# Kernel tuning notes

Hardware: AMD Instinct MI355X
Metric: run time of the kernel (lower is better)

Reference implementation:

```python
import jax, jax.numpy as jnp
import numpy as np

NUM_HEADS = 64
HEAD_DIM = 10  # forced by nn.Linear(10, 1)


def setup_inputs() -> dict:
    key = jax.random.key(0)
    kq, kk, kv, kw = jax.random.split(key, 4)
    B, T, M = 16, 4096, NUM_HEADS * HEAD_DIM
    return {
        "query": jax.random.normal(kq, (B, T, M), dtype=jnp.float32),
        "key": jax.random.normal(kk, (B, T, M), dtype=jnp.float32),
        "value": jax.random.normal(kv, (B, T, M), dtype=jnp.float32),
        "W": jax.random.normal(kw, (1, HEAD_DIM), dtype=jnp.float32) * 0.3,
        "b": jnp.zeros((1,), dtype=jnp.float32),
    }


def _to_heads(x):
    # torch: stack(split(x, head_dim, dim=2), dim=0) -> [H, B, T, D]
    B, T, M = x.shape
    return x.reshape(B, T, NUM_HEADS, HEAD_DIM).transpose(2, 0, 1, 3)


def reference(query, key, value, W, b):
    D = HEAD_DIM
    q = _to_heads(query)   # [H,B,T,D]
    k = _to_heads(key)     # [H,B,T,D]
    v = _to_heads(value)   # [H,B,T,D]
    # key.transpose(-1,-2).sum(3).unsqueeze(2): sum over T -> [H,B,1,D]
    k_sum = k.sum(axis=2, keepdims=True)
    attn = jax.nn.softmax(jnp.tanh(q * k_sum / np.float32(np.sqrt(D))), axis=-1)
    t = attn * v                          # [H,B,T,D]
    v_q = t.sum(axis=2)                   # [H,B,D]
    v_v = t.sum(axis=3).transpose(1, 0, 2)  # [B,H,T]
    # input_proj: Linear(10,1) on v_q*v_q (v_query == v_key == t summed over T)
    s = jnp.tanh((v_q * v_q) @ W.T + b)   # [H,B,1]
    s = jax.nn.softmax(s, axis=-1)        # softmax over size-1 dim (== ones)
    s = s.transpose(1, 0, 2)              # [B,H,1]
    return v_v * s                        # [B,H,T]
```

## Files before the change

### kernel.cpp

```cpp
#include <hip/hip_runtime.h>

#define BB 16
#define TT 4096
#define HH 64
#define DD 10
#define MM 640

#define TROWS 16
#define PADF  161

__global__ void zero_ws_kernel(float* __restrict__ ws, int n) {
    int i = blockIdx.x * blockDim.x + threadIdx.x;
    if (i < n) ws[i] = 0.0f;
}

__global__ void __launch_bounds__(256)
ksum_kernel(const float* __restrict__ key, float* __restrict__ ksum) {
    int g = blockIdx.x * blockDim.x + threadIdx.x;
    int b = g / 160;
    int c = g % 160;
    int t0 = blockIdx.y * 32;

    const float4* p = reinterpret_cast<const float4*>(key)
                    + (size_t)b * TT * 160 + (size_t)t0 * 160 + c;

    float4 a0 = make_float4(0.f,0.f,0.f,0.f);
    float4 a1 = make_float4(0.f,0.f,0.f,0.f);
    float4 a2 = make_float4(0.f,0.f,0.f,0.f);
    float4 a3 = make_float4(0.f,0.f,0.f,0.f);
    #pragma unroll
    for (int i = 0; i < 32; i += 4) {
        float4 x0 = p[(size_t)(i + 0) * 160];
        float4 x1 = p[(size_t)(i + 1) * 160];
        float4 x2 = p[(size_t)(i + 2) * 160];
        float4 x3 = p[(size_t)(i + 3) * 160];
        a0.x += x0.x; a0.y += x0.y; a0.z += x0.z; a0.w += x0.w;
        a1.x += x1.x; a1.y += x1.y; a1.z += x1.z; a1.w += x1.w;
        a2.x += x2.x; a2.y += x2.y; a2.z += x2.z; a2.w += x2.w;
        a3.x += x3.x; a3.y += x3.y; a3.z += x3.z; a3.w += x3.w;
    }
    float sx = (a0.x + a1.x) + (a2.x + a3.x);
    float sy = (a0.y + a1.y) + (a2.y + a3.y);
    float sz = (a0.z + a1.z) + (a2.z + a3.z);
    float sw = (a0.w + a1.w) + (a2.w + a3.w);

    float* dst = ksum + b * MM + c * 4;
    atomicAdd(dst + 0, sx);
    atomicAdd(dst + 1, sy);
    atomicAdd(dst + 2, sz);
    atomicAdd(dst + 3, sw);
}

__device__ __forceinline__ float tanh_fast(float x) {
    float ax = fabsf(x);
    float e2 = __expf(-2.0f * ax);
    float th = (1.0f - e2) / (1.0f + e2);
    return copysignf(th, x);
}

__global__ void __launch_bounds__(128)
attn_kernel(const float* __restrict__ q,
            const float* __restrict__ v,
            const float* __restrict__ ksum,
            float* __restrict__ out) {
    __shared__ float qs[TROWS * PADF];
    __shared__ float vs[TROWS * PADF];

    const int tid = threadIdx.x;
    const int t0  = blockIdx.x * TROWS;
    const int hg  = blockIdx.y;
    const int b   = blockIdx.z;

    const float4* qg = reinterpret_cast<const float4*>(q)
                     + ((size_t)(b * TT + t0)) * 160 + hg * 40;
    const float4* vg = reinterpret_cast<const float4*>(v)
                     + ((size_t)(b * TT + t0)) * 160 + hg * 40;

    float4 rq[5], rv[5];
    #pragma unroll
    for (int i = 0; i < 5; ++i) {
        int idx = tid + 128 * i;
        int row = idx / 40;
        int c   = idx % 40;
        rq[i] = qg[(size_t)row * 160 + c];
        rv[i] = vg[(size_t)row * 160 + c];
    }
    #pragma unroll
    for (int i = 0; i < 5; ++i) {
        int idx  = tid + 128 * i;
        int row  = idx / 40;
        int c    = idx % 40;
        int base = row * PADF + c * 4;
        qs[base + 0] = rq[i].x; qs[base + 1] = rq[i].y;
        qs[base + 2] = rq[i].z; qs[base + 3] = rq[i].w;
        vs[base + 0] = rv[i].x; vs[base + 1] = rv[i].y;
        vs[base + 2] = rv[i].z; vs[base + 3] = rv[i].w;
    }
    __syncthreads();

    const float R = 0.316227766016838f;
    #pragma unroll
    for (int o = 0; o < 2; ++o) {
        int p    = tid + o * 128;
        int row  = p & (TROWS - 1);
        int head = p >> 4;
        const float* ks = ksum + b * MM + hg * 160 + head * 10;

        int lbase = row * PADF + head * 10;
        float sum = 0.f, dot = 0.f;
        #pragma unroll
        for (int d = 0; d < 10; ++d) {
            float e = __expf(tanh_fast(qs[lbase + d] * ks[d] * R));
            sum += e;
            dot += e * vs[lbase + d];
        }
        out[((size_t)(b * HH + hg * 16 + head)) * TT + t0 + row] = dot / sum;
    }
}

extern "C" void kernel_launch(void* const* d_in, const int* in_sizes, int n_in,
                              void* d_out, int out_size, void* d_ws, size_t ws_size,
                              hipStream_t stream) {
    const float* q = (const float*)d_in[0];
    const float* k = (const float*)d_in[1];
    const float* v = (const float*)d_in[2];
    float* out  = (float*)d_out;
    float* ksum = (float*)d_ws;

    zero_ws_kernel<<<dim3((BB * MM + 255) / 256), dim3(256), 0, stream>>>(ksum, BB * MM);
    ksum_kernel<<<dim3(10, 128), dim3(256), 0, stream>>>(k, ksum);
    attn_kernel<<<dim3(TT / TROWS, 4, BB), dim3(128), 0, stream>>>(q, v, ksum, out);
}
```

Before: 115.8 us.

## Make attention kernel persistent with register prefetch of next tile

Turns the attention kernel into a persistent grid of a fixed number of blocks that loop over tiles. Each block prefetches the next tile's q/v into registers while it computes the current one. Shared memory is now stored as float4 rows, ksum is loaded as float2, and divisions become hardware reciprocals. The aim is to overlap global loads with compute and cut launch/tail overhead, in exchange for an extra barrier per tile and lower occupancy from held registers.

```diff
diff --git a/kernel.cpp b/kernel.cpp
--- a/kernel.cpp
+++ b/kernel.cpp
@@ -7,7 +7,9 @@
 #define MM 640
 
 #define TROWS 16
-#define PADF  161
+#define PADF4 41
+#define NBLK 1792
+#define NTILE (256 * 4 * BB)
 
 __global__ void zero_ws_kernel(float* __restrict__ ws, int n) {
     int i = blockIdx.x * blockDim.x + threadIdx.x;
@@ -51,10 +53,10 @@
     atomicAdd(dst + 3, sw);
 }
 
-__device__ __forceinline__ float tanh_fast(float x) {
+__device__ __forceinline__ float tanh_rcp(float x) {
     float ax = fabsf(x);
     float e2 = __expf(-2.0f * ax);
-    float th = (1.0f - e2) / (1.0f + e2);
+    float th = (1.0f - e2) * __builtin_amdgcn_rcpf(1.0f + e2);
     return copysignf(th, x);
 }
 
@@ -63,58 +65,96 @@
             const float* __restrict__ v,
             const float* __restrict__ ksum,
             float* __restrict__ out) {
-    __shared__ float qs[TROWS * PADF];
-    __shared__ float vs[TROWS * PADF];
+    __shared__ float4 qs[TROWS * PADF4];
+    __shared__ float4 vs[TROWS * PADF4];
 
     const int tid = threadIdx.x;
-    const int t0  = blockIdx.x * TROWS;
-    const int hg  = blockIdx.y;
-    const int b   = blockIdx.z;
+    const int bid = blockIdx.x;
 
-    const float4* qg = reinterpret_cast<const float4*>(q)
-                     + ((size_t)(b * TT + t0)) * 160 + hg * 40;
-    const float4* vg = reinterpret_cast<const float4*>(v)
-                     + ((size_t)(b * TT + t0)) * 160 + hg * 40;
-
-    float4 rq[5], rv[5];
+    int rows[5], cols[5];
     #pragma unroll
     for (int i = 0; i < 5; ++i) {
         int idx = tid + 128 * i;
-        int row = idx / 40;
-        int c   = idx % 40;
-        rq[i] = qg[(size_t)row * 160 + c];
-        rv[i] = vg[(size_t)row * 160 + c];
+        rows[i] = idx / 40;
+        cols[i] = idx % 40;
     }
-    #pragma unroll
-    for (int i = 0; i < 5; ++i) {
-        int idx  = tid + 128 * i;
-        int row  = idx / 40;
-        int c    = idx % 40;
-        int base = row * PADF + c * 4;
-        qs[base + 0] = rq[i].x; qs[base + 1] = rq[i].y;
-        qs[base + 2] = rq[i].z; qs[base + 3] = rq[i].w;
-        vs[base + 0] = rv[i].x; vs[base + 1] = rv[i].y;
-        vs[base + 2] = rv[i].z; vs[base + 3] = rv[i].w;
-    }
-    __syncthreads();
+    const int head0 = tid >> 4;
+    const int row   = tid & 15;
 
     const float R = 0.316227766016838f;
-    #pragma unroll
-    for (int o = 0; o < 2; ++o) {
-        int p    = tid + o * 128;
-        int row  = p & (TROWS - 1);
-        int head = p >> 4;
-        const float* ks = ksum + b * MM + hg * 160 + head * 10;
 
-        int lbase = row * PADF + head * 10;
-        float sum = 0.f, dot = 0.f;
+    float4 rq[5], rv[5];
+    {
+        int t0 = (bid & 255) * TROWS;
+        int hg = (bid >> 8) & 3;
+        int b  = bid >> 10;
+        const float4* qg = reinterpret_cast<const float4*>(q)
+                         + ((size_t)(b * TT + t0)) * 160 + hg * 40;
+        const float4* vg = reinterpret_cast<const float4*>(v)
+                         + ((size_t)(b * TT + t0)) * 160 + hg * 40;
         #pragma unroll
-        for (int d = 0; d < 10; ++d) {
-            float e = __expf(tanh_fast(qs[lbase + d] * ks[d] * R));
-            sum += e;
-            dot += e * vs[lbase + d];
+        for (int i = 0; i < 5; ++i) {
+            rq[i] = qg[(size_t)rows[i] * 160 + cols[i]];
+            rv[i] = vg[(size_t)rows[i] * 160 + cols[i]];
         }
-        out[((size_t)(b * HH + hg * 16 + head)) * TT + t0 + row] = dot / sum;
+    }
+
+    for (int vt = bid; vt < NTILE; vt += NBLK) {
+        const int t0 = (vt & 255) * TROWS;
+        const int hg = (vt >> 8) & 3;
+        const int b  = vt >> 10;
+
+        const float* ks0 = ksum + b * MM + hg * 160 + head0 * 10;
+        const float* ks1 = ks0 + 80;
+        float2 kk0[5], kk1[5];
+        #pragma unroll
+        for (int i = 0; i < 5; ++i) {
+            kk0[i] = *reinterpret_cast<const float2*>(ks0 + 2 * i);
+            kk1[i] = *reinterpret_cast<const float2*>(ks1 + 2 * i);
+        }
+
+        __syncthreads();
+        #pragma unroll
+        for (int i = 0; i < 5; ++i) {
+            qs[rows[i] * PADF4 + cols[i]] = rq[i];
+            vs[rows[i] * PADF4 + cols[i]] = rv[i];
+        }
+        __syncthreads();
+
+        int vn = vt + NBLK;
+        if (vn < NTILE) {
+            int t0n = (vn & 255) * TROWS;
+            int hgn = (vn >> 8) & 3;
+            int bn  = vn >> 10;
+            const float4* qg = reinterpret_cast<const float4*>(q)
+                             + ((size_t)(bn * TT + t0n)) * 160 + hgn * 40;
+            const float4* vg = reinterpret_cast<const float4*>(v)
+                             + ((size_t)(bn * TT + t0n)) * 160 + hgn * 40;
+            #pragma unroll
+            for (int i = 0; i < 5; ++i) {
+                rq[i] = qg[(size_t)rows[i] * 160 + cols[i]];
+                rv[i] = vg[(size_t)rows[i] * 160 + cols[i]];
+            }
+        }
+
+        const float* qsf = reinterpret_cast<const float*>(qs);
+        const float* vsf = reinterpret_cast<const float*>(vs);
+        #pragma unroll
+        for (int o = 0; o < 2; ++o) {
+            const int head  = head0 + o * 8;
+            const int lbase = row * (PADF4 * 4) + head * 10;
+            const float2* kk = o ? kk1 : kk0;
+            float sum = 0.f, dot = 0.f;
+            #pragma unroll
+            for (int i = 0; i < 5; ++i) {
+                float e0 = __expf(tanh_rcp(qsf[lbase + 2*i]     * kk[i].x * R));
+                float e1 = __expf(tanh_rcp(qsf[lbase + 2*i + 1] * kk[i].y * R));
+                sum += e0 + e1;
+                dot += e0 * vsf[lbase + 2*i] + e1 * vsf[lbase + 2*i + 1];
+            }
+            out[((size_t)(b * HH + hg * 16 + head)) * TT + t0 + row]
+                = dot * __builtin_amdgcn_rcpf(sum);
+        }
     }
 }
 
@@ -129,5 +169,5 @@
 
     zero_ws_kernel<<<dim3((BB * MM + 255) / 256), dim3(256), 0, stream>>>(ksum, BB * MM);
     ksum_kernel<<<dim3(10, 128), dim3(256), 0, stream>>>(k, ksum);
-    attn_kernel<<<dim3(TT / TROWS, 4, BB), dim3(128), 0, stream>>>(q, v, ksum, out);
+    attn_kernel<<<dim3(NBLK), dim3(128), 0, stream>>>(q, v, ksum, out);
 }
```

Result: slower. 200.2 us (+72.8%).

## Make attention kernel persistent with double-buffered async global-to-LDS loads

Applied to the files above, without the earlier changes.

Replaces the one-tile-per-block attention kernel with 2048 persistent single-wave blocks. Each block loops over 8-row time tiles and double-buffers q and v tiles into LDS through global_load_lds async copies, using an XOR-swizzled layout to avoid bank conflicts. The ksum values are hoisted into registers once per block, and divisions are replaced with hardware reciprocals. The aim is to overlap memory fetch with compute and cut per-block launch and sync overhead. In exchange it relies on hand-placed vmcnt waits and there is no barrier between the waves' LDS use (single wave, so it holds).

```diff
diff --git a/kernel.cpp b/kernel.cpp
--- a/kernel.cpp
+++ b/kernel.cpp
@@ -1,13 +1,15 @@
 #include <hip/hip_runtime.h>
+#include <stdint.h>
 
 #define BB 16
 #define TT 4096
 #define HH 64
-#define DD 10
 #define MM 640
 
-#define TROWS 16
-#define PADF  161
+#define TROWS 8
+#define NTT   (TT / TROWS)
+#define SUBS  32
+#define NBLK  (64 * SUBS)
 
 __global__ void zero_ws_kernel(float* __restrict__ ws, int n) {
     int i = blockIdx.x * blockDim.x + threadIdx.x;
@@ -51,70 +53,109 @@
     atomicAdd(dst + 3, sw);
 }
 
-__device__ __forceinline__ float tanh_fast(float x) {
+__device__ __forceinline__ float tanh_rcp(float x) {
     float ax = fabsf(x);
     float e2 = __expf(-2.0f * ax);
-    float th = (1.0f - e2) / (1.0f + e2);
+    float th = (1.0f - e2) * __builtin_amdgcn_rcpf(1.0f + e2);
     return copysignf(th, x);
 }
 
-__global__ void __launch_bounds__(128)
+__device__ __forceinline__ void async_cp16(const float4* g, void* l) {
+    __builtin_amdgcn_global_load_lds(
+        (const __attribute__((address_space(1))) uint32_t*)g,
+        (__attribute__((address_space(3))) uint32_t*)l,
+        16, 0, 0);
+}
+
+__global__ void __launch_bounds__(64)
 attn_kernel(const float* __restrict__ q,
             const float* __restrict__ v,
             const float* __restrict__ ksum,
             float* __restrict__ out) {
-    __shared__ float qs[TROWS * PADF];
-    __shared__ float vs[TROWS * PADF];
+    __shared__ float4 lds[2][640];
 
-    const int tid = threadIdx.x;
-    const int t0  = blockIdx.x * TROWS;
-    const int hg  = blockIdx.y;
-    const int b   = blockIdx.z;
+    const int lane = threadIdx.x;
+    const int bid  = blockIdx.x;
+    const int sub   = bid & (SUBS - 1);
+    const int combo = bid >> 5;
+    const int b  = combo >> 2;
+    const int hg = combo & 3;
 
-    const float4* qg = reinterpret_cast<const float4*>(q)
-                     + ((size_t)(b * TT + t0)) * 160 + hg * 40;
-    const float4* vg = reinterpret_cast<const float4*>(v)
-                     + ((size_t)(b * TT + t0)) * 160 + hg * 40;
-
-    float4 rq[5], rv[5];
+    int srcoff[5];
     #pragma unroll
     for (int i = 0; i < 5; ++i) {
-        int idx = tid + 128 * i;
-        int row = idx / 40;
-        int c   = idx % 40;
-        rq[i] = qg[(size_t)row * 160 + c];
-        rv[i] = vg[(size_t)row * 160 + c];
+        int s = i * 64 + lane;
+        int r = s / 40;
+        srcoff[i] = r * 160 + ((s % 40) ^ r);
     }
-    #pragma unroll
-    for (int i = 0; i < 5; ++i) {
-        int idx  = tid + 128 * i;
-        int row  = idx / 40;
-        int c    = idx % 40;
-        int base = row * PADF + c * 4;
-        qs[base + 0] = rq[i].x; qs[base + 1] = rq[i].y;
-        qs[base + 2] = rq[i].z; qs[base + 3] = rq[i].w;
-        vs[base + 0] = rv[i].x; vs[base + 1] = rv[i].y;
-        vs[base + 2] = rv[i].z; vs[base + 3] = rv[i].w;
-    }
-    __syncthreads();
+
+    const int row   = lane & 7;
+    const int head0 = lane >> 3;
+
+    const float4* qbase = (const float4*)q + (size_t)b * TT * 160 + hg * 40;
+    const float4* vbase = (const float4*)v + (size_t)b * TT * 160 + hg * 40;
 
     const float R = 0.316227766016838f;
+    float ksr[2][10];
     #pragma unroll
     for (int o = 0; o < 2; ++o) {
-        int p    = tid + o * 128;
-        int row  = p & (TROWS - 1);
-        int head = p >> 4;
-        const float* ks = ksum + b * MM + hg * 160 + head * 10;
+        const float* ks = ksum + b * MM + hg * 160 + (head0 + 8 * o) * 10;
+        #pragma unroll
+        for (int d = 0; d < 10; ++d) ksr[o][d] = ks[d] * R;
+    }
 
-        int lbase = row * PADF + head * 10;
-        float sum = 0.f, dot = 0.f;
+    float* obase0 = out + ((size_t)(b * HH + hg * 16 + head0)) * TT + row;
+    float* obase1 = obase0 + (size_t)8 * TT;
+
+    {
+        const float4* qt = qbase + (size_t)sub * 1280;
+        const float4* vt = vbase + (size_t)sub * 1280;
         #pragma unroll
-        for (int d = 0; d < 10; ++d) {
-            float e = __expf(tanh_fast(qs[lbase + d] * ks[d] * R));
-            sum += e;
-            dot += e * vs[lbase + d];
+        for (int i = 0; i < 5; ++i)
+            async_cp16(qt + srcoff[i], (char*)&lds[0][0] + i * 1024);
+        #pragma unroll
+        for (int i = 0; i < 5; ++i)
+            async_cp16(vt + srcoff[i], (char*)&lds[0][320] + i * 1024);
+    }
+
+    int buf = 0;
+    for (int tt = sub; tt < NTT; tt += SUBS) {
+        int ttn = tt + SUBS;
+        if (ttn < NTT) {
+            const float4* qt = qbase + (size_t)ttn * 1280;
+            const float4* vt = vbase + (size_t)ttn * 1280;
+            #pragma unroll
+            for (int i = 0; i < 5; ++i)
+                async_cp16(qt + srcoff[i], (char*)&lds[buf ^ 1][0] + i * 1024);
+            #pragma unroll
+            for (int i = 0; i < 5; ++i)
+                async_cp16(vt + srcoff[i], (char*)&lds[buf ^ 1][320] + i * 1024);
+            asm volatile("s_waitcnt vmcnt(10)" ::: "memory");
+        } else {
+            asm volatile("s_waitcnt vmcnt(0)" ::: "memory");
         }
-        out[((size_t)(b * HH + hg * 16 + head)) * TT + t0 + row] = dot / sum;
+        __builtin_amdgcn_sched_barrier(0);
+
+        const float* qf = (const float*)&lds[buf][0];
+        const float* vf = (const float*)&lds[buf][320];
+        const int rb = row * 160;
+        const int rx = row << 2;
+
+        #pragma unroll
+        for (int o = 0; o < 2; ++o) {
+            const int c0 = (head0 + 8 * o) * 10;
+            float sum = 0.f, dot = 0.f;
+            #pragma unroll
+            for (int d = 0; d < 10; ++d) {
+                int fi = rb + ((c0 + d) ^ rx);
+                float e = __expf(tanh_rcp(qf[fi] * ksr[o][d]));
+                sum += e;
+                dot += e * vf[fi];
+            }
+            float res = dot * __builtin_amdgcn_rcpf(sum);
+            (o ? obase1 : obase0)[(size_t)tt * TROWS] = res;
+        }
+        buf ^= 1;
     }
 }
 
@@ -129,5 +170,5 @@
 
     zero_ws_kernel<<<dim3((BB * MM + 255) / 256), dim3(256), 0, stream>>>(ksum, BB * MM);
     ksum_kernel<<<dim3(10, 128), dim3(256), 0, stream>>>(k, ksum);
-    attn_kernel<<<dim3(TT / TROWS, 4, BB), dim3(128), 0, stream>>>(q, v, ksum, out);
+    attn_kernel<<<dim3(NBLK), dim3(64), 0, stream>>>(q, v, ksum, out);
 }
```

Result: slower. 131.0 us (+13.1%).

## Make attention kernel persistent over time tiles with register-prefetch pipelining

Applied to the files above, without the earlier changes.

The attention kernel now launches 1024 blocks of 256 threads. Each block loops over 16 time tiles and prefetches the next tile of q and v into registers while it computes the current tile from shared memory. Each thread loads its ksum values once, pre-scaled, and divisions are replaced with rcp intrinsics. The workspace zero kernel becomes hipMemsetAsync. Fewer, longer blocks cut launch overhead and the repeated ksum loads, but lower parallelism and extra barriers may limit latency hiding.

```diff
diff --git a/kernel.cpp b/kernel.cpp
--- a/kernel.cpp
+++ b/kernel.cpp
@@ -1,18 +1,17 @@
 #include <hip/hip_runtime.h>
+#include <stdint.h>
 
 #define BB 16
 #define TT 4096
 #define HH 64
-#define DD 10
 #define MM 640
 
-#define TROWS 16
-#define PADF  161
-
-__global__ void zero_ws_kernel(float* __restrict__ ws, int n) {
-    int i = blockIdx.x * blockDim.x + threadIdx.x;
-    if (i < n) ws[i] = 0.0f;
-}
+#define PAD4  41
+#define ROWSF (PAD4 * 4)
+#define QVOFF (16 * ROWSF)
+#define NPART 16
+#define NITER 16
+#define NBLK  (64 * NPART)
 
 __global__ void __launch_bounds__(256)
 ksum_kernel(const float* __restrict__ key, float* __restrict__ ksum) {
@@ -51,70 +50,103 @@
     atomicAdd(dst + 3, sw);
 }
 
-__device__ __forceinline__ float tanh_fast(float x) {
+__device__ __forceinline__ float tanh_rcp(float x) {
     float ax = fabsf(x);
     float e2 = __expf(-2.0f * ax);
-    float th = (1.0f - e2) / (1.0f + e2);
+    float th = (1.0f - e2) * __builtin_amdgcn_rcpf(1.0f + e2);
     return copysignf(th, x);
 }
 
-__global__ void __launch_bounds__(128)
+__global__ void __launch_bounds__(256)
 attn_kernel(const float* __restrict__ q,
             const float* __restrict__ v,
             const float* __restrict__ ksum,
             float* __restrict__ out) {
-    __shared__ float qs[TROWS * PADF];
-    __shared__ float vs[TROWS * PADF];
+    __shared__ float sbuf[2 * 16 * ROWSF];
 
-    const int tid = threadIdx.x;
-    const int t0  = blockIdx.x * TROWS;
-    const int hg  = blockIdx.y;
-    const int b   = blockIdx.z;
+    const int tid   = threadIdx.x;
+    const int bid   = blockIdx.x;
+    const int combo = bid >> 4;
+    const int tpart = bid & (NPART - 1);
+    const int b  = combo >> 2;
+    const int hg = combo & 3;
 
-    const float4* qg = reinterpret_cast<const float4*>(q)
-                     + ((size_t)(b * TT + t0)) * 160 + hg * 40;
-    const float4* vg = reinterpret_cast<const float4*>(v)
-                     + ((size_t)(b * TT + t0)) * 160 + hg * 40;
-
-    float4 rq[5], rv[5];
+    int sr[5], sc[5], qsel[5];
     #pragma unroll
     for (int i = 0; i < 5; ++i) {
-        int idx = tid + 128 * i;
-        int row = idx / 40;
-        int c   = idx % 40;
-        rq[i] = qg[(size_t)row * 160 + c];
-        rv[i] = vg[(size_t)row * 160 + c];
+        int idx = tid + 256 * i;
+        int qq  = (idx < 640) ? 1 : 0;
+        int s   = qq ? idx : (idx - 640);
+        sr[i] = s / 40;
+        sc[i] = s % 40;
+        qsel[i] = qq;
+    }
+
+    const int row  = tid & 15;
+    const int head = tid >> 4;
+
+    const float R = 0.316227766016838f;
+    float ksr[10];
+    {
+        const float* ks = ksum + b * MM + hg * 160 + head * 10;
+        #pragma unroll
+        for (int d = 0; d < 10; ++d) ksr[d] = ks[d] * R;
+    }
+
+    const float4* qb4 = (const float4*)q + (size_t)b * TT * 160 + hg * 40;
+    const float4* vb4 = (const float4*)v + (size_t)b * TT * 160 + hg * 40;
+    float* ob = out + ((size_t)(b * HH + hg * 16 + head)) * TT + row;
+
+    float4  rs[5];
+    float4* s4 = (float4*)sbuf;
+    const int tbase = tpart * (NITER * 16);
+
+    #pragma unroll
+    for (int i = 0; i < 5; ++i) {
+        const float4* base = qsel[i] ? qb4 : vb4;
+        rs[i] = base[(size_t)(tbase + sr[i]) * 160 + sc[i]];
     }
     #pragma unroll
-    for (int i = 0; i < 5; ++i) {
-        int idx  = tid + 128 * i;
-        int row  = idx / 40;
-        int c    = idx % 40;
-        int base = row * PADF + c * 4;
-        qs[base + 0] = rq[i].x; qs[base + 1] = rq[i].y;
-        qs[base + 2] = rq[i].z; qs[base + 3] = rq[i].w;
-        vs[base + 0] = rv[i].x; vs[base + 1] = rv[i].y;
-        vs[base + 2] = rv[i].z; vs[base + 3] = rv[i].w;
-    }
-    __syncthreads();
+    for (int i = 0; i < 5; ++i)
+        s4[(qsel[i] ? 0 : 656) + sr[i] * PAD4 + sc[i]] = rs[i];
+    asm volatile("s_waitcnt lgkmcnt(0)" ::: "memory");
+    __builtin_amdgcn_s_barrier();
+    __builtin_amdgcn_sched_barrier(0);
 
-    const float R = 0.316227766016838f;
-    #pragma unroll
-    for (int o = 0; o < 2; ++o) {
-        int p    = tid + o * 128;
-        int row  = p & (TROWS - 1);
-        int head = p >> 4;
-        const float* ks = ksum + b * MM + hg * 160 + head * 10;
+    for (int it = 0; it < NITER; ++it) {
+        const int trow0 = tbase + it * 16;
 
-        int lbase = row * PADF + head * 10;
+        if (it + 1 < NITER) {
+            const int trn = trow0 + 16;
+            #pragma unroll
+            for (int i = 0; i < 5; ++i) {
+                const float4* base = qsel[i] ? qb4 : vb4;
+                rs[i] = base[(size_t)(trn + sr[i]) * 160 + sc[i]];
+            }
+        }
+        __builtin_amdgcn_sched_barrier(0);
+
+        const int fb = row * ROWSF + head * 10;
         float sum = 0.f, dot = 0.f;
         #pragma unroll
         for (int d = 0; d < 10; ++d) {
-            float e = __expf(tanh_fast(qs[lbase + d] * ks[d] * R));
+            float e = __expf(tanh_rcp(sbuf[fb + d] * ksr[d]));
             sum += e;
-            dot += e * vs[lbase + d];
+            dot += e * sbuf[QVOFF + fb + d];
         }
-        out[((size_t)(b * HH + hg * 16 + head)) * TT + t0 + row] = dot / sum;
+        ob[trow0] = dot * __builtin_amdgcn_rcpf(sum);
+
+        __builtin_amdgcn_sched_barrier(0);
+        __builtin_amdgcn_s_barrier();
+
+        if (it + 1 < NITER) {
+            #pragma unroll
+            for (int i = 0; i < 5; ++i)
+                s4[(qsel[i] ? 0 : 656) + sr[i] * PAD4 + sc[i]] = rs[i];
+            asm volatile("s_waitcnt lgkmcnt(0)" ::: "memory");
+            __builtin_amdgcn_s_barrier();
+            __builtin_amdgcn_sched_barrier(0);
+        }
     }
 }
 
@@ -127,7 +159,7 @@
     float* out  = (float*)d_out;
     float* ksum = (float*)d_ws;
 
-    zero_ws_kernel<<<dim3((BB * MM + 255) / 256), dim3(256), 0, stream>>>(ksum, BB * MM);
+    hipMemsetAsync(d_ws, 0, (size_t)BB * MM * sizeof(float), stream);
     ksum_kernel<<<dim3(10, 128), dim3(256), 0, stream>>>(k, ksum);
-    attn_kernel<<<dim3(TT / TROWS, 4, BB), dim3(128), 0, stream>>>(q, v, ksum, out);
+    attn_kernel<<<dim3(NBLK), dim3(256), 0, stream>>>(q, v, ksum, out);
 }
```

Result: slower. 153.4 us (+32.4%).
